# Kernel tuning notes

Hardware: AMD Instinct MI355X
Metric: run time of the kernel (lower is better)

The kernel has to match this reference:

```python
import jax, jax.numpy as jnp
import numpy as np

# Static module config (matches init_kwargs, world_size=1)
DIM = 256
HEADS = 8
HD = DIM // HEADS            # 32
WS = (8, 8)                  # window_size
DS = (2, 2)                  # dilated_size
SH = (4, 4)                  # shift_size
TW = (WS[0] * DS[0], WS[1] * DS[1])  # total_window_size (16,16)
SCALE = HD ** (-0.5)
N = WS[0] * WS[1]            # tokens per attention group = 64


def _rope2(t):
    # 2D rotary embedding on a (G, wh, ww, HD) grid: first half of channels
    # rotated by the h position, second half by the w position.
    G, wh, ww, hd = t.shape
    da = hd // 2
    half = da // 2
    inv = 1.0 / (10000.0 ** (jnp.arange(half, dtype=jnp.float32) / half))

    def cs(n):
        ang = jnp.arange(n, dtype=jnp.float32)[:, None] * inv  # (n, half)
        return jnp.cos(ang), jnp.sin(ang)

    cH, sH = cs(wh)
    cW, sW = cs(ww)

    def rot(u, c, s):  # rotate-half style rotation
        u1, u2 = u[..., :half], u[..., half:]
        return jnp.concatenate([u1 * c - u2 * s, u1 * s + u2 * c], axis=-1)

    th = rot(t[..., :da], cH[None, :, None, :], sH[None, :, None, :])
    tw = rot(t[..., da:], cW[None, None, :, :], sW[None, None, :, :])
    return jnp.concatenate([th, tw], axis=-1)


def _build_mask(H, W):
    # Faithful replication of create_mask (2D branch), done in numpy since
    # H, W are static under jit.
    img = np.zeros((H, W), dtype=np.float32)
    h_sl = (slice(0, -WS[0]), slice(-WS[0], -SH[0]), slice(-SH[0], None))
    w_sl = (slice(0, -WS[1]), slice(-WS[1], 0), slice(0, None))
    cnt = 0
    for hs in h_sl:
        for wsl in w_sl:
            img[hs, wsl] = cnt
            cnt += 1
    nH, nW = H // TW[0], W // TW[1]
    # window_partition with total_window_size
    mw = img.reshape(nH, TW[0], nW, TW[1]).transpose(0, 2, 1, 3).reshape(-1, TW[0], TW[1])
    Bm = mw.shape[0]
    # window_partition with dilated_size + regroup by dilation offset
    mw = (mw.reshape(Bm, WS[0], DS[0], WS[1], DS[1])
            .transpose(0, 1, 3, 2, 4)
            .reshape(Bm, N, DS[0] * DS[1])
            .transpose(0, 2, 1)
            .reshape(Bm * DS[0] * DS[1], N))
    am = np.where(mw[:, None, :] != mw[:, :, None], -np.inf, 0.0).astype(np.float32)
    return jnp.asarray(am)  # (nWm, N, N)


def reference(x, W_qkv, b_qkv, W_proj, b_proj):
    Bs, H, W, C = x.shape
    nH, nW = H // TW[0], W // TW[1]
    nWm = nH * nW * DS[0] * DS[1]
    B_ = Bs * nWm
    Bwin = Bs * nH * nW

    mask = _build_mask(H, W)  # (nWm, N, N) additive 0/-inf

    # qkv projection (ColumnParallelLinear, world_size=1)
    qkv = x.reshape(Bs * H * W, C) @ W_qkv + b_qkv  # (Bs*H*W, 3C)

    # NOTE: the original forward computes shifted/partitioned qkv_windows but
    # then reshapes the UNshifted raster-order qkv for q,k,v (replicated here).
    qkv = qkv.reshape(B_, N, 3, HEADS, HD).transpose(2, 0, 3, 1, 4)  # (3,B_,h,N,hd)
    q, k, v = qkv[0], qkv[1], qkv[2]

    q = _rope2(q.reshape(-1, WS[0], WS[1], HD)).reshape(B_, HEADS, N, HD)
    k = _rope2(k.reshape(-1, WS[0], WS[1], HD)).reshape(B_, HEADS, N, HD)

    attn = jnp.einsum('bhnd,bhmd->bhnm', q * SCALE, k)  # (B_,h,N,N)
    attn = attn.reshape(Bs, nWm, HEADS, N, N) + mask[None, :, None, :, :]
    attn = jax.nn.softmax(attn, axis=-1).reshape(B_, HEADS, N, N)

    out = jnp.einsum('bhnm,bhmd->bhnd', attn, v)           # (B_,h,N,hd)
    out = out.transpose(0, 2, 1, 3).reshape(B_, N, C)      # (B_,N,C)

    # undo dilation regrouping: (Bwin, d0*d1, N, C) -> (Bwin, N, d0*d1, C)
    out = out.reshape(Bwin, DS[0] * DS[1], N, C).transpose(0, 2, 1, 3)
    # window_reverse over dilated blocks -> (Bwin, TW0, TW1, C)
    out = (out.reshape(Bwin, WS[0], WS[1], DS[0], DS[1], C)
              .transpose(0, 1, 3, 2, 4, 5)
              .reshape(Bwin, TW[0], TW[1], C))
    # window_reverse over total windows -> (Bs, H, W, C)
    out = (out.reshape(Bs, nH, nW, TW[0], TW[1], C)
              .transpose(0, 1, 3, 2, 4, 5)
              .reshape(Bs, H, W, C))

    # roll back (shift_size[0] > 0 branch)
    out = jnp.roll(out, shift=(SH[0], SH[1]), axis=(1, 2))

    # output projection (RowParallelLinear, world_size=1)
    out = out.reshape(Bs * H * W, C) @ W_proj + b_proj
    return out.reshape(Bs, H, W, C)


def setup_inputs() -> dict:
    key = jax.random.key(0)
    k1, k2, k3 = jax.random.split(key, 3)
    x = jax.random.normal(k1, (4, 192, 192, DIM), dtype=jnp.float32)
    W_qkv = jax.random.normal(k2, (DIM, 3 * DIM), dtype=jnp.float32) * 0.02
    b_qkv = jnp.zeros((3 * DIM,), dtype=jnp.float32)
    W_proj = jax.random.normal(k3, (DIM, DIM), dtype=jnp.float32) * 0.02
    b_proj = jnp.zeros((DIM,), dtype=jnp.float32)
    return {'x': x, 'W_qkv': W_qkv, 'b_qkv': b_qkv, 'W_proj': W_proj, 'b_proj': b_proj}
```

## Files before the change

kernel.cpp:

```cpp
#include <hip/hip_runtime.h>
#include <hip/hip_bf16.h>
#include <cstdint>

static constexpr int MROWS = 147456;
static constexpr int KDIM  = 256;
static constexpr int QKVN  = 768;

typedef __bf16 bf16x8 __attribute__((ext_vector_type(8)));
typedef float  f32x4  __attribute__((ext_vector_type(4)));

static __device__ __forceinline__ uint16_t f2bf(float f) {
    uint32_t x = __float_as_uint(f);
    x += 0x7FFFu + ((x >> 16) & 1u);
    return (uint16_t)(x >> 16);
}
static __device__ __forceinline__ float bl(uint32_t u) { return __uint_as_float(u << 16); }
static __device__ __forceinline__ float bh(uint32_t u) { return __uint_as_float(u & 0xffff0000u); }
static __device__ __forceinline__ uint32_t pack2(float a, float b) {
    return (uint32_t)f2bf(a) | ((uint32_t)f2bf(b) << 16);
}

__global__ void cvt_f32_bf16_k(const float* __restrict__ in, uint16_t* __restrict__ out, int n4)
{
    int i = blockIdx.x * blockDim.x + threadIdx.x;
    const int stride = gridDim.x * blockDim.x;
    for (; i < n4; i += stride) {
        float4 v = ((const float4*)in)[i];
        uint2 o;
        o.x = pack2(v.x, v.y);
        o.y = pack2(v.z, v.w);
        ((uint2*)out)[i] = o;
    }
}

__global__ void transpose_cvt_k(const float* __restrict__ W, uint16_t* __restrict__ Wt, int K, int N)
{
    int id = blockIdx.x * blockDim.x + threadIdx.x;
    if (id >= K * N) return;
    int n = id / K, k = id - n * K;
    Wt[id] = f2bf(W[(size_t)k * N + n]);
}

template<int OUT_BF16>
__global__ __launch_bounds__(256)
void gemm_bf16(const uint16_t* __restrict__ A, const uint16_t* __restrict__ Bt,
               const float* __restrict__ bias, void* __restrict__ Cout,
               int M, int N, int K, int ntn)
{
    __shared__ __align__(16) uint16_t lds[2][2][128 * 32];

    const int tid = threadIdx.x;
    const int wv = tid >> 6, ln = tid & 63;

    const int nwg = gridDim.x;
    const int q8 = nwg >> 3;
    const int sw = (blockIdx.x & 7) * q8 + (blockIdx.x >> 3);
    const int bm = (sw / ntn) * 128;
    const int bn = (sw - (sw / ntn) * ntn) * 128;

    const uint16_t* Ab = A + (size_t)bm * K;
    const uint16_t* Bb = Bt + (size_t)bn * K;

    const int wr = (wv >> 1) * 64;
    const int wc = (wv & 1) * 64;
    const int frow = ln & 15;
    const int kb = (ln >> 4) * 16;

    f32x4 acc[4][4] = {};

    auto stage = [&](int buf, int k0) {
        #pragma unroll
        for (int it = 0; it < 2; ++it) {
            const int c = it * 256 + wv * 64 + ln;
            const int row = c >> 2, kl = c & 3;
            const int ks = kl ^ ((row ^ (row >> 2)) & 3);
            const uint16_t* srcA = Ab + row * K + k0 + ks * 8;
            const uint16_t* srcB = Bb + row * K + k0 + ks * 8;
            uint16_t* dA = &lds[buf][0][(size_t)(it * 256 + wv * 64) * 8];
            uint16_t* dB = &lds[buf][1][(size_t)(it * 256 + wv * 64) * 8];
            __builtin_amdgcn_global_load_lds((const __attribute__((address_space(1))) void*)srcA,
                                             (__attribute__((address_space(3))) void*)dA, 16, 0, 0);
            __builtin_amdgcn_global_load_lds((const __attribute__((address_space(1))) void*)srcB,
                                             (__attribute__((address_space(3))) void*)dB, 16, 0, 0);
        }
    };

    stage(0, 0);
    const int nt = K / 32;
    for (int t = 0; t < nt; ++t) {
        const int cur = t & 1;
        __syncthreads();
        if (t + 1 < nt) stage(cur ^ 1, (t + 1) * 32);
        bf16x8 af[4], bfr[4];
        #pragma unroll
        for (int i = 0; i < 4; ++i) {
            const int rA = wr + i * 16 + frow;
            const int offA = (rA * 64 + kb) ^ (((rA ^ (rA >> 2)) & 3) << 4);
            af[i] = *(const bf16x8*)((const char*)&lds[cur][0][0] + offA);
            const int rB = wc + i * 16 + frow;
            const int offB = (rB * 64 + kb) ^ (((rB ^ (rB >> 2)) & 3) << 4);
            bfr[i] = *(const bf16x8*)((const char*)&lds[cur][1][0] + offB);
        }
        #pragma unroll
        for (int i = 0; i < 4; ++i)
            #pragma unroll
            for (int j = 0; j < 4; ++j)
                acc[i][j] = __builtin_amdgcn_mfma_f32_16x16x32_bf16(af[i], bfr[j], acc[i][j], 0, 0, 0);
    }

    const int r4 = (ln >> 4) * 4;
    #pragma unroll
    for (int i = 0; i < 4; ++i) {
        #pragma unroll
        for (int j = 0; j < 4; ++j) {
            const int col = bn + wc + j * 16 + frow;
            const float bs = bias[col];
            #pragma unroll
            for (int r = 0; r < 4; ++r) {
                const int row = bm + wr + i * 16 + r4 + r;
                const float v = acc[i][j][r] + bs;
                if (OUT_BF16) ((uint16_t*)Cout)[(size_t)row * N + col] = f2bf(v);
                else          ((float*)Cout)[(size_t)row * N + col]    = v;
            }
        }
    }
}

__global__ __launch_bounds__(64)
void attn_win_mfma(const uint16_t* __restrict__ qkv, uint16_t* __restrict__ out2)
{
    __shared__ __align__(16) uint16_t lds[7424];

    const int bid  = blockIdx.x;
    const int b_   = bid >> 3;
    const int head = bid & 7;
    const int n    = threadIdx.x;
    const int wh   = n >> 3;
    const int wwp  = n & 7;
    const int frow = n & 15;
    const int hi4  = n >> 4;
    const int fk   = hi4 * 8;
    const int r4   = hi4 * 4;

    const uint16_t* rowp = qkv + (size_t)(b_ * 64 + n) * 768 + head * 32;

    float q[32], kr[32];
    uint4 vraw[4];
    #pragma unroll
    for (int i = 0; i < 4; ++i) {
        uint4 t = *(const uint4*)(rowp + i * 8);
        q[i*8+0] = bl(t.x); q[i*8+1] = bh(t.x);
        q[i*8+2] = bl(t.y); q[i*8+3] = bh(t.y);
        q[i*8+4] = bl(t.z); q[i*8+5] = bh(t.z);
        q[i*8+6] = bl(t.w); q[i*8+7] = bh(t.w);
    }
    #pragma unroll
    for (int i = 0; i < 4; ++i) {
        uint4 t = *(const uint4*)(rowp + 256 + i * 8);
        kr[i*8+0] = bl(t.x); kr[i*8+1] = bh(t.x);
        kr[i*8+2] = bl(t.y); kr[i*8+3] = bh(t.y);
        kr[i*8+4] = bl(t.z); kr[i*8+5] = bh(t.z);
        kr[i*8+6] = bl(t.w); kr[i*8+7] = bh(t.w);
    }
    #pragma unroll
    for (int i = 0; i < 4; ++i) vraw[i] = *(const uint4*)(rowp + 512 + i * 8);

    const float SCALE = 0.17677669529663687f;
    #pragma unroll
    for (int j = 0; j < 8; ++j) {
        const float invj = __expf(-1.1512925464970231f * (float)j);
        float sH, cH, sW, cW;
        __sincosf((float)wh  * invj, &sH, &cH);
        __sincosf((float)wwp * invj, &sW, &cW);
        float u1, u2;
        u1 = q[j];      u2 = q[j + 8];   q[j]      = u1*cH - u2*sH;  q[j + 8]   = u1*sH + u2*cH;
        u1 = q[16 + j]; u2 = q[24 + j];  q[16 + j] = u1*cW - u2*sW;  q[24 + j]  = u1*sW + u2*cW;
        u1 = kr[j];      u2 = kr[j + 8];   kr[j]      = u1*cH - u2*sH;  kr[j + 8]  = u1*sH + u2*cH;
        u1 = kr[16 + j]; u2 = kr[24 + j];  kr[16 + j] = u1*cW - u2*sW;  kr[24 + j] = u1*sW + u2*cW;
    }

    #pragma unroll
    for (int i = 0; i < 4; ++i) {
        uint4 t;
        t.x = pack2(q[i*8+0]*SCALE, q[i*8+1]*SCALE);
        t.y = pack2(q[i*8+2]*SCALE, q[i*8+3]*SCALE);
        t.z = pack2(q[i*8+4]*SCALE, q[i*8+5]*SCALE);
        t.w = pack2(q[i*8+6]*SCALE, q[i*8+7]*SCALE);
        *(uint4*)&lds[n * 40 + i * 8] = t;
        uint4 u;
        u.x = pack2(kr[i*8+0], kr[i*8+1]);
        u.y = pack2(kr[i*8+2], kr[i*8+3]);
        u.z = pack2(kr[i*8+4], kr[i*8+5]);
        u.w = pack2(kr[i*8+6], kr[i*8+7]);
        *(uint4*)&lds[2560 + n * 40 + i * 8] = u;
    }
    #pragma unroll
    for (int i = 0; i < 4; ++i) {
        lds[5120 + (i*8+0) * 72 + n] = (uint16_t)(vraw[i].x & 0xffff);
        lds[5120 + (i*8+1) * 72 + n] = (uint16_t)(vraw[i].x >> 16);
        lds[5120 + (i*8+2) * 72 + n] = (uint16_t)(vraw[i].y & 0xffff);
        lds[5120 + (i*8+3) * 72 + n] = (uint16_t)(vraw[i].y >> 16);
        lds[5120 + (i*8+4) * 72 + n] = (uint16_t)(vraw[i].z & 0xffff);
        lds[5120 + (i*8+5) * 72 + n] = (uint16_t)(vraw[i].z >> 16);
        lds[5120 + (i*8+6) * 72 + n] = (uint16_t)(vraw[i].w & 0xffff);
        lds[5120 + (i*8+7) * 72 + n] = (uint16_t)(vraw[i].w >> 16);
    }
    __syncthreads();

    bf16x8 qf[4], kf[4];
    #pragma unroll
    for (int i = 0; i < 4; ++i) {
        qf[i] = *(const bf16x8*)&lds[(16 * i + frow) * 40 + fk];
        kf[i] = *(const bf16x8*)&lds[2560 + (16 * i + frow) * 40 + fk];
    }
    f32x4 s[4][4] = {};
    #pragma unroll
    for (int i = 0; i < 4; ++i)
        #pragma unroll
        for (int j = 0; j < 4; ++j)
            s[i][j] = __builtin_amdgcn_mfma_f32_16x16x32_bf16(qf[i], kf[j], s[i][j], 0, 0, 0);

    float p[4][4][4];
    #pragma unroll
    for (int i = 0; i < 4; ++i)
        #pragma unroll
        for (int j = 0; j < 4; ++j)
            #pragma unroll
            for (int r = 0; r < 4; ++r)
                p[i][j][r] = __expf(s[i][j][r]);

    const int wm = b_ % 576;
    if (wm >= 528) {
        int kc[4];
        #pragma unroll
        for (int j = 0; j < 4; ++j) {
            const int kh = (16 * j + frow) >> 3;
            kc[j] = (kh < 4) ? 0 : ((kh < 6) ? 1 : 2);
        }
        #pragma unroll
        for (int i = 0; i < 4; ++i)
            #pragma unroll
            for (int r = 0; r < 4; ++r) {
                const int qh = (16 * i + r4 + r) >> 3;
                const int qc = (qh < 4) ? 0 : ((qh < 6) ? 1 : 2);
                #pragma unroll
                for (int j = 0; j < 4; ++j)
                    if (kc[j] != qc) p[i][j][r] = 0.f;
            }
    }

    float rinv[4][4];
    #pragma unroll
    for (int i = 0; i < 4; ++i)
        #pragma unroll
        for (int r = 0; r < 4; ++r) {
            float sum = p[i][0][r] + p[i][1][r] + p[i][2][r] + p[i][3][r];
            sum += __shfl_xor(sum, 1);
            sum += __shfl_xor(sum, 2);
            sum += __shfl_xor(sum, 4);
            sum += __shfl_xor(sum, 8);
            rinv[i][r] = 1.f / sum;
        }

    __syncthreads();
    #pragma unroll
    for (int i = 0; i < 4; ++i)
        #pragma unroll
        for (int r = 0; r < 4; ++r)
            #pragma unroll
            for (int j = 0; j < 4; ++j)
                lds[(16 * i + r4 + r) * 72 + 16 * j + frow] = f2bf(p[i][j][r]);
    __syncthreads();

    bf16x8 pf[4][2], vf[2][2];
    #pragma unroll
    for (int i = 0; i < 4; ++i)
        #pragma unroll
        for (int kc = 0; kc < 2; ++kc)
            pf[i][kc] = *(const bf16x8*)&lds[(16 * i + frow) * 72 + kc * 32 + fk];
    #pragma unroll
    for (int jv = 0; jv < 2; ++jv)
        #pragma unroll
        for (int kc = 0; kc < 2; ++kc)
            vf[jv][kc] = *(const bf16x8*)&lds[5120 + (16 * jv + frow) * 72 + kc * 32 + fk];

    f32x4 o[4][2] = {};
    #pragma unroll
    for (int i = 0; i < 4; ++i)
        #pragma unroll
        for (int jv = 0; jv < 2; ++jv) {
            o[i][jv] = __builtin_amdgcn_mfma_f32_16x16x32_bf16(pf[i][0], vf[jv][0], o[i][jv], 0, 0, 0);
            o[i][jv] = __builtin_amdgcn_mfma_f32_16x16x32_bf16(pf[i][1], vf[jv][1], o[i][jv], 0, 0, 0);
        }

    __syncthreads();
    #pragma unroll
    for (int i = 0; i < 4; ++i)
        #pragma unroll
        for (int jv = 0; jv < 2; ++jv)
            #pragma unroll
            for (int r = 0; r < 4; ++r)
                lds[(16 * i + r4 + r) * 40 + 16 * jv + frow] = f2bf(o[i][jv][r] * rinv[i][r]);
    __syncthreads();

    const int bw = b_ >> 2, ds = b_ & 3, dh = ds >> 1, dw = ds & 1;
    const int bimg = bw / 144;
    const int t144 = bw % 144;
    const int bh = t144 / 12, bwc = t144 % 12;
    int hp = bh * 16 + wh * 2 + dh + 4;  if (hp >= 192) hp -= 192;
    int wp = bwc * 16 + wwp * 2 + dw + 4; if (wp >= 192) wp -= 192;

    uint16_t* dst = out2 + ((size_t)(bimg * 192 + hp) * 192 + wp) * 256 + head * 32;
    #pragma unroll
    for (int i = 0; i < 4; ++i)
        *(uint4*)(dst + i * 8) = *(const uint4*)&lds[n * 40 + i * 8];
}

extern "C" void kernel_launch(void* const* d_in, const int* in_sizes, int n_in,
                              void* d_out, int out_size, void* d_ws, size_t ws_size,
                              hipStream_t stream)
{
    const float* x      = (const float*)d_in[0];
    const float* W_qkv  = (const float*)d_in[1];
    const float* b_qkv  = (const float*)d_in[2];
    const float* W_proj = (const float*)d_in[3];
    const float* b_proj = (const float*)d_in[4];
    float* out = (float*)d_out;

    uint16_t* xb   = (uint16_t*)d_ws;
    uint16_t* qkvb = xb   + (size_t)MROWS * KDIM;
    uint16_t* bufb = qkvb + (size_t)MROWS * QKVN;
    uint16_t* wtq  = bufb + (size_t)MROWS * KDIM;
    uint16_t* wtp  = wtq  + (size_t)QKVN * KDIM;

    cvt_f32_bf16_k<<<2048, 256, 0, stream>>>(x, xb, MROWS * KDIM / 4);
    transpose_cvt_k<<<(KDIM * QKVN + 255) / 256, 256, 0, stream>>>(W_qkv, wtq, KDIM, QKVN);
    transpose_cvt_k<<<(KDIM * KDIM + 255) / 256, 256, 0, stream>>>(W_proj, wtp, KDIM, KDIM);

    gemm_bf16<1><<<(MROWS / 128) * (QKVN / 128), 256, 0, stream>>>(
        xb, wtq, b_qkv, qkvb, MROWS, QKVN, KDIM, QKVN / 128);

    attn_win_mfma<<<2304 * 8, 64, 0, stream>>>(qkvb, bufb);

    gemm_bf16<0><<<(MROWS / 128) * (KDIM / 128), 256, 0, stream>>>(
        bufb, wtp, b_proj, out, MROWS, KDIM, KDIM, KDIM / 128);
}
```

Measured before the change: 344.1 us.

## Fuse input conversion, QKV projection, RoPE and window attention into one kernel

Replaces the separate fp32-to-bf16 conversion, QKV GEMM and per-head attention kernels with one kernel. Each 256-thread block loads a 64-token group of x, converts it in LDS, and computes the QKV projection for four heads with MFMA, streaming per-head-block weights through LDS. It then applies bias, RoPE and scaling in registers and runs attention, one wave per head. This removes the round-trip of the bf16 x and the large QKV intermediate through global memory. In exchange, weights are re-read for every window group, LDS use is high, there are more barriers, and softmax normalisation now happens before P·V in bf16.

```diff
diff --git a/kernel.cpp b/kernel.cpp
--- a/kernel.cpp
+++ b/kernel.cpp
@@ -4,7 +4,6 @@
 
 static constexpr int MROWS = 147456;
 static constexpr int KDIM  = 256;
-static constexpr int QKVN  = 768;
 
 typedef __bf16 bf16x8 __attribute__((ext_vector_type(8)));
 typedef float  f32x4  __attribute__((ext_vector_type(4)));
@@ -14,23 +13,35 @@
     x += 0x7FFFu + ((x >> 16) & 1u);
     return (uint16_t)(x >> 16);
 }
-static __device__ __forceinline__ float bl(uint32_t u) { return __uint_as_float(u << 16); }
-static __device__ __forceinline__ float bh(uint32_t u) { return __uint_as_float(u & 0xffff0000u); }
 static __device__ __forceinline__ uint32_t pack2(float a, float b) {
     return (uint32_t)f2bf(a) | ((uint32_t)f2bf(b) << 16);
 }
 
-__global__ void cvt_f32_bf16_k(const float* __restrict__ in, uint16_t* __restrict__ out, int n4)
-{
-    int i = blockIdx.x * blockDim.x + threadIdx.x;
-    const int stride = gridDim.x * blockDim.x;
-    for (; i < n4; i += stride) {
-        float4 v = ((const float4*)in)[i];
-        uint2 o;
-        o.x = pack2(v.x, v.y);
-        o.y = pack2(v.z, v.w);
-        ((uint2*)out)[i] = o;
-    }
+static __device__ __forceinline__ int gcol(int hb, int j) {
+    if (j < 128) return hb * 128 + j;
+    if (j < 256) return 256 + hb * 128 + (j - 128);
+    return 512 + hb * 128 + (j - 256);
+}
+
+__global__ void build_wb(const float* __restrict__ Wqkv, uint16_t* __restrict__ Wb)
+{
+    int id = blockIdx.x * blockDim.x + threadIdx.x;
+    if (id >= 2 * 8 * 384 * 32) return;
+    int kk = id & 31;
+    int tmp = id >> 5;
+    int j = tmp % 384;
+    int ht = tmp / 384;
+    int t = ht & 7, hb = ht >> 3;
+    int k = t * 32 + kk;
+    Wb[id] = f2bf(Wqkv[(size_t)k * 768 + gcol(hb, j)]);
+}
+
+__global__ void build_biasb(const float* __restrict__ bq, float* __restrict__ biasb)
+{
+    int id = blockIdx.x * blockDim.x + threadIdx.x;
+    if (id >= 768) return;
+    int hb = id / 384, j = id % 384;
+    biasb[id] = bq[gcol(hb, j)];
 }
 
 __global__ void transpose_cvt_k(const float* __restrict__ W, uint16_t* __restrict__ Wt, int K, int N)
@@ -126,92 +137,121 @@
     }
 }
 
-__global__ __launch_bounds__(64)
-void attn_win_mfma(const uint16_t* __restrict__ qkv, uint16_t* __restrict__ out2)
-{
-    __shared__ __align__(16) uint16_t lds[7424];
-
-    const int bid  = blockIdx.x;
-    const int b_   = bid >> 3;
-    const int head = bid & 7;
-    const int n    = threadIdx.x;
-    const int wh   = n >> 3;
-    const int wwp  = n & 7;
-    const int frow = n & 15;
-    const int hi4  = n >> 4;
-    const int fk   = hi4 * 8;
-    const int r4   = hi4 * 4;
-
-    const uint16_t* rowp = qkv + (size_t)(b_ * 64 + n) * 768 + head * 32;
-
-    float q[32], kr[32];
-    uint4 vraw[4];
+__global__ __launch_bounds__(256, 2)
+void fused_qkv_attn(const float* __restrict__ x, const uint16_t* __restrict__ Wb,
+                    const float* __restrict__ biasb, uint16_t* __restrict__ out2)
+{
+    __shared__ __align__(16) uint16_t lds[29184];
+    uint16_t* R0 = lds;
+    uint16_t* R1 = lds + 16896;
+
+    const int tid = threadIdx.x;
+    const int wv = tid >> 6, ln = tid & 63;
+    const int frow = ln & 15, hi4 = ln >> 4;
+    const int fk = hi4 * 8, r4 = hi4 * 4;
+
+    const int nb = gridDim.x;
+    const int sw = (blockIdx.x & 7) * (nb >> 3) + (blockIdx.x >> 3);
+    const int b_ = sw >> 1, hb = sw & 1;
+
+    const float4* xs = (const float4*)(x + (size_t)b_ * 64 * 256);
+    const uint16_t* Wblk = Wb + (size_t)hb * 8 * 12288;
+
+    uint4 wr[6];
+    #pragma unroll
+    for (int it = 0; it < 6; ++it)
+        wr[it] = *(const uint4*)(Wblk + (it * 256 + tid) * 8);
+
+    #pragma unroll
+    for (int it = 0; it < 8; ++it) {
+        const int idx8 = it * 256 + tid;
+        float4 a = xs[idx8 * 2], b = xs[idx8 * 2 + 1];
+        uint4 o;
+        o.x = pack2(a.x, a.y); o.y = pack2(a.z, a.w);
+        o.z = pack2(b.x, b.y); o.w = pack2(b.z, b.w);
+        *(uint4*)&R0[(idx8 >> 5) * 264 + (idx8 & 31) * 8] = o;
+    }
+    #pragma unroll
+    for (int it = 0; it < 6; ++it)
+        *(uint4*)&R1[(it * 256 + tid) * 8] = wr[it];
+    __syncthreads();
+
+    f32x4 acc[4][6] = {};
+    for (int t = 0; t < 8; ++t) {
+        if (t < 7) {
+            const uint16_t* Ws = Wblk + (size_t)(t + 1) * 12288;
+            #pragma unroll
+            for (int it = 0; it < 6; ++it)
+                wr[it] = *(const uint4*)(Ws + (it * 256 + tid) * 8);
+        }
+        bf16x8 af[4], bfr[6];
+        #pragma unroll
+        for (int i = 0; i < 4; ++i)
+            af[i] = *(const bf16x8*)&R0[(16 * i + frow) * 264 + t * 32 + fk];
+        #pragma unroll
+        for (int j = 0; j < 6; ++j)
+            bfr[j] = *(const bf16x8*)&R1[(wv * 96 + 16 * j + frow) * 32 + fk];
+        #pragma unroll
+        for (int i = 0; i < 4; ++i)
+            #pragma unroll
+            for (int j = 0; j < 6; ++j)
+                acc[i][j] = __builtin_amdgcn_mfma_f32_16x16x32_bf16(af[i], bfr[j], acc[i][j], 0, 0, 0);
+        if (t < 7) {
+            __syncthreads();
+            #pragma unroll
+            for (int it = 0; it < 6; ++it)
+                *(uint4*)&R1[(it * 256 + tid) * 8] = wr[it];
+            __syncthreads();
+        }
+    }
+    __syncthreads();
+
+    const float SCALE = 0.17677669529663687f;
+    const float invf = __expf(-1.1512925464970231f * (float)(frow & 7));
+    const float sgn = (frow & 8) ? 1.f : -1.f;
+
+    #pragma unroll
+    for (int j = 0; j < 6; ++j) {
+        const int g = wv * 6 + j;
+        const float bs = biasb[hb * 384 + g * 16 + frow];
+        if (g < 16) {
+            const int half = g & 1;
+            #pragma unroll
+            for (int i = 0; i < 4; ++i) {
+                #pragma unroll
+                for (int r = 0; r < 4; ++r) {
+                    const int row = 16 * i + r4 + r;
+                    const int pos = half ? (row & 7) : (row >> 3);
+                    float sv, cv;
+                    __sincosf((float)pos * invf, &sv, &cv);
+                    float v = acc[i][j][r] + bs;
+                    float part = __shfl_xor(v, 8);
+                    float nv = v * cv + sgn * part * sv;
+                    if (g < 8) nv *= SCALE;
+                    float pp = __shfl_xor(nv, 1);
+                    if (!(frow & 1))
+                        *(uint32_t*)&R0[row * 264 + g * 16 + frow] = pack2(nv, pp);
+                }
+            }
+        } else {
+            const int vh = (g - 16) >> 1;
+            const int d = (g & 1) * 16 + frow;
+            #pragma unroll
+            for (int i = 0; i < 4; ++i)
+                #pragma unroll
+                for (int r = 0; r < 4; ++r) {
+                    const int row = 16 * i + r4 + r;
+                    R1[vh * 2304 + d * 72 + row] = f2bf(acc[i][j][r] + bs);
+                }
+        }
+    }
+    __syncthreads();
+
+    bf16x8 qf[4], kf[4];
     #pragma unroll
     for (int i = 0; i < 4; ++i) {
-        uint4 t = *(const uint4*)(rowp + i * 8);
-        q[i*8+0] = bl(t.x); q[i*8+1] = bh(t.x);
-        q[i*8+2] = bl(t.y); q[i*8+3] = bh(t.y);
-        q[i*8+4] = bl(t.z); q[i*8+5] = bh(t.z);
-        q[i*8+6] = bl(t.w); q[i*8+7] = bh(t.w);
-    }
-    #pragma unroll
-    for (int i = 0; i < 4; ++i) {
-        uint4 t = *(const uint4*)(rowp + 256 + i * 8);
-        kr[i*8+0] = bl(t.x); kr[i*8+1] = bh(t.x);
-        kr[i*8+2] = bl(t.y); kr[i*8+3] = bh(t.y);
-        kr[i*8+4] = bl(t.z); kr[i*8+5] = bh(t.z);
-        kr[i*8+6] = bl(t.w); kr[i*8+7] = bh(t.w);
-    }
-    #pragma unroll
-    for (int i = 0; i < 4; ++i) vraw[i] = *(const uint4*)(rowp + 512 + i * 8);
-
-    const float SCALE = 0.17677669529663687f;
-    #pragma unroll
-    for (int j = 0; j < 8; ++j) {
-        const float invj = __expf(-1.1512925464970231f * (float)j);
-        float sH, cH, sW, cW;
-        __sincosf((float)wh  * invj, &sH, &cH);
-        __sincosf((float)wwp * invj, &sW, &cW);
-        float u1, u2;
-        u1 = q[j];      u2 = q[j + 8];   q[j]      = u1*cH - u2*sH;  q[j + 8]   = u1*sH + u2*cH;
-        u1 = q[16 + j]; u2 = q[24 + j];  q[16 + j] = u1*cW - u2*sW;  q[24 + j]  = u1*sW + u2*cW;
-        u1 = kr[j];      u2 = kr[j + 8];   kr[j]      = u1*cH - u2*sH;  kr[j + 8]  = u1*sH + u2*cH;
-        u1 = kr[16 + j]; u2 = kr[24 + j];  kr[16 + j] = u1*cW - u2*sW;  kr[24 + j] = u1*sW + u2*cW;
-    }
-
-    #pragma unroll
-    for (int i = 0; i < 4; ++i) {
-        uint4 t;
-        t.x = pack2(q[i*8+0]*SCALE, q[i*8+1]*SCALE);
-        t.y = pack2(q[i*8+2]*SCALE, q[i*8+3]*SCALE);
-        t.z = pack2(q[i*8+4]*SCALE, q[i*8+5]*SCALE);
-        t.w = pack2(q[i*8+6]*SCALE, q[i*8+7]*SCALE);
-        *(uint4*)&lds[n * 40 + i * 8] = t;
-        uint4 u;
-        u.x = pack2(kr[i*8+0], kr[i*8+1]);
-        u.y = pack2(kr[i*8+2], kr[i*8+3]);
-        u.z = pack2(kr[i*8+4], kr[i*8+5]);
-        u.w = pack2(kr[i*8+6], kr[i*8+7]);
-        *(uint4*)&lds[2560 + n * 40 + i * 8] = u;
-    }
-    #pragma unroll
-    for (int i = 0; i < 4; ++i) {
-        lds[5120 + (i*8+0) * 72 + n] = (uint16_t)(vraw[i].x & 0xffff);
-        lds[5120 + (i*8+1) * 72 + n] = (uint16_t)(vraw[i].x >> 16);
-        lds[5120 + (i*8+2) * 72 + n] = (uint16_t)(vraw[i].y & 0xffff);
-        lds[5120 + (i*8+3) * 72 + n] = (uint16_t)(vraw[i].y >> 16);
-        lds[5120 + (i*8+4) * 72 + n] = (uint16_t)(vraw[i].z & 0xffff);
-        lds[5120 + (i*8+5) * 72 + n] = (uint16_t)(vraw[i].z >> 16);
-        lds[5120 + (i*8+6) * 72 + n] = (uint16_t)(vraw[i].w & 0xffff);
-        lds[5120 + (i*8+7) * 72 + n] = (uint16_t)(vraw[i].w >> 16);
-    }
-    __syncthreads();
-
-    bf16x8 qf[4], kf[4];
-    #pragma unroll
-    for (int i = 0; i < 4; ++i) {
-        qf[i] = *(const bf16x8*)&lds[(16 * i + frow) * 40 + fk];
-        kf[i] = *(const bf16x8*)&lds[2560 + (16 * i + frow) * 40 + fk];
+        qf[i] = *(const bf16x8*)&R0[(16 * i + frow) * 264 + wv * 32 + fk];
+        kf[i] = *(const bf16x8*)&R0[(16 * i + frow) * 264 + 128 + wv * 32 + fk];
     }
     f32x4 s[4][4] = {};
     #pragma unroll
@@ -231,11 +271,11 @@
 
     const int wm = b_ % 576;
     if (wm >= 528) {
-        int kc[4];
+        int kcls[4];
         #pragma unroll
         for (int j = 0; j < 4; ++j) {
             const int kh = (16 * j + frow) >> 3;
-            kc[j] = (kh < 4) ? 0 : ((kh < 6) ? 1 : 2);
+            kcls[j] = (kh < 4) ? 0 : ((kh < 6) ? 1 : 2);
         }
         #pragma unroll
         for (int i = 0; i < 4; ++i)
@@ -245,7 +285,7 @@
                 const int qc = (qh < 4) ? 0 : ((qh < 6) ? 1 : 2);
                 #pragma unroll
                 for (int j = 0; j < 4; ++j)
-                    if (kc[j] != qc) p[i][j][r] = 0.f;
+                    if (kcls[j] != qc) p[i][j][r] = 0.f;
             }
     }
 
@@ -266,10 +306,17 @@
     #pragma unroll
     for (int i = 0; i < 4; ++i)
         #pragma unroll
-        for (int r = 0; r < 4; ++r)
-            #pragma unroll
-            for (int j = 0; j < 4; ++j)
-                lds[(16 * i + r4 + r) * 72 + 16 * j + frow] = f2bf(p[i][j][r]);
+        for (int r = 0; r < 4; ++r) {
+            const float sc = rinv[i][r];
+            const int row = 16 * i + r4 + r;
+            #pragma unroll
+            for (int j = 0; j < 4; ++j) {
+                float pv = p[i][j][r] * sc;
+                float pp = __shfl_xor(pv, 1);
+                if (!(frow & 1))
+                    *(uint32_t*)&R0[row * 264 + wv * 64 + 16 * j + frow] = pack2(pv, pp);
+            }
+        }
     __syncthreads();
 
     bf16x8 pf[4][2], vf[2][2];
@@ -277,12 +324,13 @@
     for (int i = 0; i < 4; ++i)
         #pragma unroll
         for (int kc = 0; kc < 2; ++kc)
-            pf[i][kc] = *(const bf16x8*)&lds[(16 * i + frow) * 72 + kc * 32 + fk];
+            pf[i][kc] = *(const bf16x8*)&R0[(16 * i + frow) * 264 + wv * 64 + kc * 32 + fk];
     #pragma unroll
     for (int jv = 0; jv < 2; ++jv)
         #pragma unroll
         for (int kc = 0; kc < 2; ++kc)
-            vf[jv][kc] = *(const bf16x8*)&lds[5120 + (16 * jv + frow) * 72 + kc * 32 + fk];
+            vf[jv][kc] = *(const bf16x8*)&R1[wv * 2304 + (16 * jv + frow) * 72 + kc * 32 + fk];
+    __syncthreads();
 
     f32x4 o[4][2] = {};
     #pragma unroll
@@ -293,27 +341,32 @@
             o[i][jv] = __builtin_amdgcn_mfma_f32_16x16x32_bf16(pf[i][1], vf[jv][1], o[i][jv], 0, 0, 0);
         }
 
-    __syncthreads();
     #pragma unroll
     for (int i = 0; i < 4; ++i)
         #pragma unroll
         for (int jv = 0; jv < 2; ++jv)
             #pragma unroll
-            for (int r = 0; r < 4; ++r)
-                lds[(16 * i + r4 + r) * 40 + 16 * jv + frow] = f2bf(o[i][jv][r] * rinv[i][r]);
-    __syncthreads();
-
-    const int bw = b_ >> 2, ds = b_ & 3, dh = ds >> 1, dw = ds & 1;
+            for (int r = 0; r < 4; ++r) {
+                float val = o[i][jv][r];
+                float pp = __shfl_xor(val, 1);
+                if (!(frow & 1))
+                    *(uint32_t*)&R0[wv * 2560 + (16 * i + r4 + r) * 40 + 16 * jv + frow] = pack2(val, pp);
+            }
+    __syncthreads();
+
+    const int n = ln;
+    const int wh = n >> 3, wwp = n & 7;
+    const int bw = b_ >> 2, dsw = b_ & 3, dh = dsw >> 1, dw = dsw & 1;
     const int bimg = bw / 144;
     const int t144 = bw % 144;
     const int bh = t144 / 12, bwc = t144 % 12;
     int hp = bh * 16 + wh * 2 + dh + 4;  if (hp >= 192) hp -= 192;
     int wp = bwc * 16 + wwp * 2 + dw + 4; if (wp >= 192) wp -= 192;
 
-    uint16_t* dst = out2 + ((size_t)(bimg * 192 + hp) * 192 + wp) * 256 + head * 32;
-    #pragma unroll
-    for (int i = 0; i < 4; ++i)
-        *(uint4*)(dst + i * 8) = *(const uint4*)&lds[n * 40 + i * 8];
+    uint16_t* dst = out2 + ((size_t)(bimg * 192 + hp) * 192 + wp) * 256 + (hb * 4 + wv) * 32;
+    #pragma unroll
+    for (int i = 0; i < 4; ++i)
+        *(uint4*)(dst + i * 8) = *(const uint4*)&R0[wv * 2560 + n * 40 + i * 8];
 }
 
 extern "C" void kernel_launch(void* const* d_in, const int* in_sizes, int n_in,
@@ -327,20 +380,16 @@
     const float* b_proj = (const float*)d_in[4];
     float* out = (float*)d_out;
 
-    uint16_t* xb   = (uint16_t*)d_ws;
-    uint16_t* qkvb = xb   + (size_t)MROWS * KDIM;
-    uint16_t* bufb = qkvb + (size_t)MROWS * QKVN;
-    uint16_t* wtq  = bufb + (size_t)MROWS * KDIM;
-    uint16_t* wtp  = wtq  + (size_t)QKVN * KDIM;
-
-    cvt_f32_bf16_k<<<2048, 256, 0, stream>>>(x, xb, MROWS * KDIM / 4);
-    transpose_cvt_k<<<(KDIM * QKVN + 255) / 256, 256, 0, stream>>>(W_qkv, wtq, KDIM, QKVN);
+    uint16_t* bufb  = (uint16_t*)d_ws;
+    uint16_t* wtp   = bufb + (size_t)MROWS * KDIM;
+    uint16_t* Wb    = wtp + 256 * 256;
+    float*    biasb = (float*)(Wb + 196608);
+
+    build_wb<<<768, 256, 0, stream>>>(W_qkv, Wb);
+    build_biasb<<<3, 256, 0, stream>>>(b_qkv, biasb);
     transpose_cvt_k<<<(KDIM * KDIM + 255) / 256, 256, 0, stream>>>(W_proj, wtp, KDIM, KDIM);
 
-    gemm_bf16<1><<<(MROWS / 128) * (QKVN / 128), 256, 0, stream>>>(
-        xb, wtq, b_qkv, qkvb, MROWS, QKVN, KDIM, QKVN / 128);
-
-    attn_win_mfma<<<2304 * 8, 64, 0, stream>>>(qkvb, bufb);
+    fused_qkv_attn<<<4608, 256, 0, stream>>>(x, Wb, biasb, bufb);
 
     gemm_bf16<0><<<(MROWS / 128) * (KDIM / 128), 256, 0, stream>>>(
         bufb, wtp, b_proj, out, MROWS, KDIM, KDIM, KDIM / 128);
```

Result: slower. 458.7 us (+33.3%).
